# Performance work log

Measured on AMD Instinct MI355X. Metric: run time of the kernel, lower is better.

Reference implementation:

```python
import jax, jax.numpy as jnp
import numpy as np

N = 100000
E = 3200000
IN_C, HID_C, OUT_C = 128, 128, 64


def setup_inputs() -> dict:
    key = jax.random.key(0)
    k_x, k_e, k_w1, k_w2 = jax.random.split(key, 4)
    x = jax.random.normal(k_x, (N, IN_C), dtype=jnp.float32)
    edge_index = jax.random.randint(k_e, (2, E), 0, N, dtype=jnp.int64)
    # GCNConv uses Glorot-init weight [in, out] and zero bias
    W1 = jax.random.normal(k_w1, (IN_C, HID_C), dtype=jnp.float32) * (1.0 / np.sqrt(IN_C))
    b1 = jnp.zeros((HID_C,), dtype=jnp.float32)
    W2 = jax.random.normal(k_w2, (HID_C, OUT_C), dtype=jnp.float32) * (1.0 / np.sqrt(HID_C))
    b2 = jnp.zeros((OUT_C,), dtype=jnp.float32)
    return {"x": x, "edge_index": edge_index, "W1": W1, "b1": b1, "W2": W2, "b2": b2}


def _gcn_norm(edge_index, n_nodes):
    """Add self-loops and compute symmetric normalization coefficients."""
    loop = jnp.arange(n_nodes, dtype=edge_index.dtype)
    src = jnp.concatenate([edge_index[0], loop])  # [E+N]
    dst = jnp.concatenate([edge_index[1], loop])  # [E+N]
    ones = jnp.ones(src.shape[0], dtype=jnp.float32)
    deg = jax.ops.segment_sum(ones, dst, num_segments=n_nodes)  # in-degree w/ self loops
    dinv = jnp.where(deg > 0, jax.lax.rsqrt(deg), 0.0)
    norm = dinv[src] * dinv[dst]  # [E+N]
    return src, dst, norm


def _gcn_conv(x, W, b, src, dst, norm, n_nodes):
    h = x @ W                                   # [N, out] dense transform first (PyG order)
    msg = norm[:, None] * h[src]                # gather + scale  [E+N, out]
    out = jax.ops.segment_sum(msg, dst, num_segments=n_nodes)  # scatter-add
    return out + b


def reference(x, edge_index, W1, b1, W2, b2):
    src, dst, norm = _gcn_norm(edge_index, N)
    h = _gcn_conv(x, W1, b1, src, dst, norm, N)
    h = jax.nn.relu(h)
    out = _gcn_conv(h, W2, b2, src, dst, norm, N)
    return out
```

## Files before the change

### kernel.cpp

```cpp
#include <hip/hip_runtime.h>

typedef unsigned int u32;
typedef unsigned short u16;
typedef unsigned long long u64;
typedef __bf16 bf16x8 __attribute__((ext_vector_type(8)));
typedef float floatx4 __attribute__((ext_vector_type(4)));
typedef u32 u32x2 __attribute__((ext_vector_type(2)));
typedef u32 u32x4 __attribute__((ext_vector_type(4)));
typedef float floatx2 __attribute__((ext_vector_type(2)));

__device__ __forceinline__ u16 f2bf(float f) {
  u32 u = __float_as_uint(f);
  u += 0x7fffu + ((u >> 16) & 1u);
  return (u16)(u >> 16);
}
__device__ __forceinline__ float bflo(u32 v) { return __uint_as_float(v << 16); }
__device__ __forceinline__ float bfhi(u32 v) { return __uint_as_float(v & 0xffff0000u); }

#define SLICE_SH 10
#define SL (1 << SLICE_SH)
#define MAXNS 128
#define NBBIN 1280

__global__ void probe_dtypes(const u16* __restrict__ xs, const u32* __restrict__ eis,
                             int* __restrict__ flags, int* __restrict__ scur) {
  int lane = threadIdx.x;
  if (lane < MAXNS) scur[lane] = 0;
  if (lane >= 64) return;
  int big = 0;
  for (int i = lane; i < 4096; i += 64) {
    u32 e = (xs[i] >> 7) & 0xffu;
    big += (e >= 0xC0u) ? 1 : 0;
  }
  int odd = 0;
  for (int i = lane; i < 256; i += 64)
    odd += (eis[2 * i + 1] != 0u) ? 1 : 0;
#pragma unroll
  for (int off = 32; off; off >>= 1) {
    big += __shfl_down(big, off);
    odd += __shfl_down(odd, off);
  }
  if (lane == 0 && blockIdx.x == 0) {
    flags[0] = (big > 16) ? 1 : 0;
    flags[1] = (odd == 0) ? 1 : 0;
  }
}


template <int OUT, bool XPROBED>
__device__ __forceinline__ void gemm_body(const void* __restrict__ Xv,
                                          const void* __restrict__ Wv,
                                          const int* __restrict__ flags,
                                          u16* __restrict__ Y, int nrows,
                                          int bid, u16* Wt) {
  constexpr int K = 128;
  constexpr int NT = OUT / 16;
  constexpr int LDW = K + 8;
  const int wf32 = flags[0];
  const int xf32 = XPROBED ? wf32 : 0;
  int tid = threadIdx.x;
  if (wf32) {
    const float* Wf = (const float*)Wv;
    for (int idx = tid; idx < K * OUT; idx += 256) {
      int k = idx / OUT, n = idx % OUT;
      Wt[n * LDW + k] = f2bf(Wf[idx]);
    }
  } else {
    const u16* Wu = (const u16*)Wv;
    for (int idx = tid; idx < K * OUT; idx += 256) {
      int k = idx / OUT, n = idx % OUT;
      Wt[n * LDW + k] = Wu[idx];
    }
  }
  __syncthreads();
  int lane = tid & 63, wave = tid >> 6;
  int quad = lane >> 4, low = lane & 15;
  int mBase = bid * 64 + wave * 16;
  int m = mBase + low;
  int ml = (m < nrows) ? m : (nrows - 1);
  floatx4 acc[NT];
#pragma unroll
  for (int i = 0; i < NT; i++) acc[i] = (floatx4)0.0f;
#pragma unroll
  for (int kb = 0; kb < 4; kb++) {
    int k0 = kb * 32 + quad * 8;
    bf16x8 a;
    if (xf32) {
      const float* Xf = (const float*)Xv;
      floatx4 p0 = *(const floatx4*)(Xf + (size_t)ml * K + k0);
      floatx4 p1 = *(const floatx4*)(Xf + (size_t)ml * K + k0 + 4);
      union { bf16x8 v; u16 s[8]; } au;
#pragma unroll
      for (int j = 0; j < 4; j++) { au.s[j] = f2bf(p0[j]); au.s[4 + j] = f2bf(p1[j]); }
      a = au.v;
    } else {
      a = *(const bf16x8*)((const u16*)Xv + (size_t)ml * K + k0);
    }
#pragma unroll
    for (int nt = 0; nt < NT; nt++) {
      bf16x8 b = *(const bf16x8*)(&Wt[(nt * 16 + low) * LDW + k0]);
      acc[nt] = __builtin_amdgcn_mfma_f32_16x16x32_bf16(a, b, acc[nt], 0, 0, 0);
    }
  }
#pragma unroll
  for (int nt = 0; nt < NT; nt++) {
    int col = nt * 16 + low;
#pragma unroll
    for (int r = 0; r < 4; r++) {
      int row = mBase + quad * 4 + r;
      if (row < nrows) Y[(size_t)row * OUT + col] = f2bf(acc[nt][r]);
    }
  }
}

__device__ __forceinline__ void bin_body(const int* __restrict__ ei,
                                         const int* __restrict__ flags,
                                         int* __restrict__ scur,
                                         u64* __restrict__ stA, u64* __restrict__ stB,
                                         int splitS, int cap, int e, int ns,
                                         int bid, int* hist, int* curs) {
  int per = (e + NBBIN - 1) / NBBIN;
  int e0 = bid * per;
  int e1 = e0 + per; if (e1 > e) e1 = e;
  const int i64f = flags[1];
  for (int t = threadIdx.x; t < ns; t += 256) hist[t] = 0;
  __syncthreads();
  for (int i = e0 + threadIdx.x; i < e1; i += 256) {
    int d = i64f ? ei[2 * (e + i)] : ei[e + i];
    atomicAdd(&hist[d >> SLICE_SH], 1);
  }
  __syncthreads();
  for (int t = threadIdx.x; t < ns; t += 256)
    curs[t] = atomicAdd(&scur[t], hist[t]);
  __syncthreads();
  int i = e0 + threadIdx.x;
  for (; i + 768 < e1; i += 1024) {
    int d[4], s[4], pos[4];
#pragma unroll
    for (int p = 0; p < 4; p++) {
      int ii = i + 256 * p;
      if (i64f) { s[p] = ei[2 * ii]; d[p] = ei[2 * (e + ii)]; }
      else      { s[p] = ei[ii];     d[p] = ei[e + ii]; }
    }
#pragma unroll
    for (int p = 0; p < 4; p++) pos[p] = atomicAdd(&curs[d[p] >> SLICE_SH], 1);
#pragma unroll
    for (int p = 0; p < 4; p++) {
      int sl = d[p] >> SLICE_SH;
      u64* st = (sl < splitS) ? stA + (size_t)sl * cap : stB + (size_t)(sl - splitS) * cap;
      st[pos[p]] = ((u64)(u32)d[p] << 32) | (u32)s[p];
    }
  }
  for (; i < e1; i += 256) {
    int s, d;
    if (i64f) { s = ei[2 * i]; d = ei[2 * (e + i)]; }
    else      { s = ei[i];     d = ei[e + i]; }
    int sl = d >> SLICE_SH;
    u64* st = (sl < splitS) ? stA + (size_t)sl * cap : stB + (size_t)(sl - splitS) * cap;
    st[atomicAdd(&curs[sl], 1)] = ((u64)(u32)d << 32) | (u32)s;
  }
}

__global__ __launch_bounds__(256) void gemm1_bin(const void* __restrict__ Xv,
                                                 const void* __restrict__ Wv,
                                                 const int* __restrict__ flags,
                                                 u16* __restrict__ Y, int nrows, int nbGemm,
                                                 const int* __restrict__ ei,
                                                 int* __restrict__ scur,
                                                 u64* __restrict__ stA, u64* __restrict__ stB,
                                                 int splitS, int cap, int e, int ns) {
  __shared__ __attribute__((aligned(16))) char smbuf[128 * 136 * 2];
  int id = blockIdx.x;
  int small = (NBBIN < nbGemm) ? NBBIN : nbGemm;
  int isBin, bid;
  if (id < 2 * small) { isBin = !(id & 1); bid = id >> 1; }
  else { bid = small + (id - 2 * small); isBin = (NBBIN > nbGemm); }
  if (isBin) {
    int* hist = (int*)smbuf;
    int* curs = hist + MAXNS;
    bin_body(ei, flags, scur, stA, stB, splitS, cap, e, ns, bid, hist, curs);
  } else {
    gemm_body<128, true>(Xv, Wv, flags, Y, nrows, bid, (u16*)smbuf);
  }
}

__global__ __launch_bounds__(256) void gemm2_k(const void* __restrict__ Xv,
                                               const void* __restrict__ Wv,
                                               const int* __restrict__ flags,
                                               u16* __restrict__ Y, int nrows) {
  __shared__ u16 Wt[64 * 136];
  gemm_body<64, false>(Xv, Wv, flags, Y, nrows, blockIdx.x, Wt);
}

__global__ __launch_bounds__(1024) void fill_slice3(const u64* __restrict__ stA,
                                                    const u64* __restrict__ stB,
                                                    const int* __restrict__ scur,
                                                    int* __restrict__ rp,
                                                    float* __restrict__ dinv,
                                                    int* __restrict__ csr,
                                                    int splitS, int cap, int n, int ns) {
  __shared__ int cnt[SL];
  __shared__ int part[SL];
  __shared__ int sb[MAXNS];
  const int s = blockIdx.x;
  const int base = s << SLICE_SH;
  const int tid = threadIdx.x;
  cnt[tid] = 0;
  if (tid < MAXNS) sb[tid] = (tid < ns) ? scur[tid] : 0;
  __syncthreads();
  for (int off = 1; off < MAXNS; off <<= 1) {
    int v = 0;
    if (tid < MAXNS && tid >= off) v = sb[tid - off];
    __syncthreads();
    if (tid < MAXNS) sb[tid] += v;
    __syncthreads();
  }
  const int csrLo = s ? sb[s - 1] : 0;
  const int m = sb[s] - csrLo;
  if (s == ns - 1 && tid == 0) rp[n] = sb[ns - 1];
  const u64* st = (s < splitS) ? stA + (size_t)s * cap : stB + (size_t)(s - splitS) * cap;
  {
    int i = tid;
    for (; i + 7168 < m; i += 8192) {
      int b[8];
#pragma unroll
      for (int p = 0; p < 8; p++) b[p] = (int)(st[i + 1024 * p] >> 32) & (SL - 1);
#pragma unroll
      for (int p = 0; p < 8; p++) atomicAdd(&cnt[b[p]], 1);
    }
    for (; i < m; i += 1024)
      atomicAdd(&cnt[(int)(st[i] >> 32) & (SL - 1)], 1);
  }
  __syncthreads();
  int c0 = cnt[tid];
  part[tid] = c0;
  __syncthreads();
  for (int off = 1; off < SL; off <<= 1) {
    int t = (tid >= off) ? part[tid - off] : 0;
    __syncthreads();
    part[tid] += t;
    __syncthreads();
  }
  int p0 = csrLo + (tid ? part[tid - 1] : 0);
  __syncthreads();
  cnt[tid] = p0;
  int d0 = base + tid;
  if (d0 < n) { rp[d0] = p0; dinv[d0] = rsqrtf((float)(c0 + 1)); }
  __syncthreads();
  {
    int i = tid;
    for (; i + 7168 < m; i += 8192) {
      u64 pr[8]; int pos[8];
#pragma unroll
      for (int p = 0; p < 8; p++) pr[p] = st[i + 1024 * p];
#pragma unroll
      for (int p = 0; p < 8; p++)
        pos[p] = atomicAdd(&cnt[(int)(pr[p] >> 32) & (SL - 1)], 1);
#pragma unroll
      for (int p = 0; p < 8; p++) csr[pos[p]] = (int)(pr[p] & 0xffffffffu);
    }
    for (; i < m; i += 1024) {
      u64 pr = st[i];
      int pos = atomicAdd(&cnt[(int)(pr >> 32) & (SL - 1)], 1);
      csr[pos] = (int)(pr & 0xffffffffu);
    }
  }
}


__global__ __launch_bounds__(256) void agg_128(const u32* __restrict__ H,
                                               const int* __restrict__ rp,
                                               const int* __restrict__ cs,
                                               const float* __restrict__ dinv,
                                               const void* __restrict__ biasv,
                                               const int* __restrict__ flags,
                                               u32* __restrict__ out, int n) {
  int node = blockIdx.x * 4 + (threadIdx.x >> 6);
  if (node >= n) return;
  int lane = threadIdx.x & 63;
  int e4 = lane >> 4, c = lane & 15;
  int s0 = rp[node], s1 = rp[node + 1];
  float a[8] = {0.f, 0.f, 0.f, 0.f, 0.f, 0.f, 0.f, 0.f};
  for (int base = s0; base < s1; base += 64) {
    int nb = s1 - base; if (nb > 64) nb = 64;
    int src = 0; float dv = 0.f;
    if (lane < nb) { src = cs[base + lane]; dv = dinv[src]; }
    for (int j = 0; j < nb; j += 16) {
      u32x4 v[4]; float w[4];
#pragma unroll
      for (int p = 0; p < 4; p++) {
        int idx = j + 4 * p + e4;
        int sj = __shfl(src, idx);
        w[p] = __shfl(dv, idx);
        v[p] = *(const u32x4*)(H + (size_t)sj * 64 + 4 * c);
      }
#pragma unroll
      for (int p = 0; p < 4; p++) {
#pragma unroll
        for (int k = 0; k < 4; k++) {
          a[2 * k]     += w[p] * bflo(v[p][k]);
          a[2 * k + 1] += w[p] * bfhi(v[p][k]);
        }
      }
    }
  }
#pragma unroll
  for (int k = 0; k < 8; k++) {
    a[k] += __shfl_xor(a[k], 16);
    a[k] += __shfl_xor(a[k], 32);
  }
  float ds = dinv[node];
  u32x4 vs = *(const u32x4*)(H + (size_t)node * 64 + 4 * c);
  float r[8];
#pragma unroll
  for (int k = 0; k < 4; k++) {
    r[2 * k]     = ds * (a[2 * k]     + ds * bflo(vs[k]));
    r[2 * k + 1] = ds * (a[2 * k + 1] + ds * bfhi(vs[k]));
  }
  if (flags[0]) {
    floatx4 b0 = *(const floatx4*)((const float*)biasv + 8 * c);
    floatx4 b1 = *(const floatx4*)((const float*)biasv + 8 * c + 4);
#pragma unroll
    for (int k = 0; k < 4; k++) { r[k] += b0[k]; r[4 + k] += b1[k]; }
  } else {
    u32x4 bb = *(const u32x4*)((const u32*)biasv + 4 * c);
#pragma unroll
    for (int k = 0; k < 4; k++) { r[2 * k] += bflo(bb[k]); r[2 * k + 1] += bfhi(bb[k]); }
  }
#pragma unroll
  for (int k = 0; k < 8; k++) r[k] = fmaxf(r[k], 0.f);
  if (e4 == 0) {
    u32x4 o;
#pragma unroll
    for (int k = 0; k < 4; k++)
      o[k] = (u32)f2bf(r[2 * k]) | ((u32)f2bf(r[2 * k + 1]) << 16);
    *(u32x4*)(out + (size_t)node * 64 + 4 * c) = o;
  }
}

__global__ __launch_bounds__(256) void agg_64(const u16* __restrict__ Hu,
                                              const int* __restrict__ rp,
                                              const int* __restrict__ cs,
                                              const float* __restrict__ dinv,
                                              const void* __restrict__ biasv,
                                              const int* __restrict__ flags,
                                              void* __restrict__ outv, int n) {
  const u32* H = (const u32*)Hu;
  int node = blockIdx.x * 4 + (threadIdx.x >> 6);
  if (node >= n) return;
  int lane = threadIdx.x & 63;
  int e4 = lane >> 4, c = lane & 15;
  int s0 = rp[node], s1 = rp[node + 1];
  float a[4] = {0.f, 0.f, 0.f, 0.f};
  for (int base = s0; base < s1; base += 64) {
    int nb = s1 - base; if (nb > 64) nb = 64;
    int src = 0; float dv = 0.f;
    if (lane < nb) { src = cs[base + lane]; dv = dinv[src]; }
    for (int j = 0; j < nb; j += 16) {
      u32x2 v[4]; float w[4];
#pragma unroll
      for (int p = 0; p < 4; p++) {
        int idx = j + 4 * p + e4;
        int sj = __shfl(src, idx);
        w[p] = __shfl(dv, idx);
        v[p] = *(const u32x2*)(H + (size_t)sj * 32 + 2 * c);
      }
#pragma unroll
      for (int p = 0; p < 4; p++) {
        a[0] += w[p] * bflo(v[p].x); a[1] += w[p] * bfhi(v[p].x);
        a[2] += w[p] * bflo(v[p].y); a[3] += w[p] * bfhi(v[p].y);
      }
    }
  }
#pragma unroll
  for (int k = 0; k < 4; k++) {
    a[k] += __shfl_xor(a[k], 16);
    a[k] += __shfl_xor(a[k], 32);
  }
  float ds = dinv[node];
  u32x2 vs = *(const u32x2*)(H + (size_t)node * 32 + 2 * c);
  float r0 = ds * (a[0] + ds * bflo(vs.x));
  float r1 = ds * (a[1] + ds * bfhi(vs.x));
  float r2 = ds * (a[2] + ds * bflo(vs.y));
  float r3 = ds * (a[3] + ds * bfhi(vs.y));
  if (flags[0]) {
    floatx4 bf = *(const floatx4*)((const float*)biasv + 4 * c);
    r0 += bf[0]; r1 += bf[1]; r2 += bf[2]; r3 += bf[3];
    if (e4 == 0) {
      floatx4 o; o[0] = r0; o[1] = r1; o[2] = r2; o[3] = r3;
      *(floatx4*)((float*)outv + (size_t)node * 64 + 4 * c) = o;
    }
  } else {
    u32x2 bb = *(const u32x2*)((const u32*)biasv + 2 * c);
    r0 += bflo(bb.x); r1 += bfhi(bb.x); r2 += bflo(bb.y); r3 += bfhi(bb.y);
    if (e4 == 0) {
      u32x2 o;
      o.x = (u32)f2bf(r0) | ((u32)f2bf(r1) << 16);
      o.y = (u32)f2bf(r2) | ((u32)f2bf(r3) << 16);
      *(u32x2*)((u32*)outv + (size_t)node * 32 + 2 * c) = o;
    }
  }
}


extern "C" void kernel_launch(void* const* d_in, const int* in_sizes, int n_in,
                              void* d_out, int out_size, void* d_ws, size_t ws_size,
                              hipStream_t stream) {
  const void* x  = d_in[0];
  const int*  ei = (const int*)d_in[1];
  const void* W1 = d_in[2];
  const void* b1 = d_in[3];
  const void* W2 = d_in[4];
  const void* b2 = d_in[5];
  const int N = in_sizes[0] / 128;
  const int E = in_sizes[1] / 2;
  const int NS = (N + SL - 1) >> SLICE_SH;

  int CAP = (E + NS - 1) / NS;
  CAP += CAP / 8;
  size_t doutSlots = ((size_t)out_size * 2) / 8;
  int SPLIT = (int)(doutSlots / (size_t)CAP);
  if (SPLIT > NS) SPLIT = NS;

  auto al = [](size_t v) { return (v + 255) & ~(size_t)255; };
  char* ws = (char*)d_ws;
  size_t o = 0;
  int*   flags = (int*)(ws + o);  o += 256;
  int*   scur  = (int*)(ws + o);  o += 512;
  int*   rp    = (int*)(ws + o);  o += al((size_t)(N + 1) * 4);
  float* dinv  = (float*)(ws + o); o += al((size_t)N * 4);
  int*   csr   = (int*)(ws + o);  o += al((size_t)E * 4);
  u16*   h     = (u16*)(ws + o);  o += al((size_t)N * 128 * 2);
  u16*   h1    = (u16*)(ws + o);  o += al((size_t)N * 128 * 2);
  u16*   h2    = h;
  u64* stA = (u64*)d_out;
  u64* stB = (u64*)h1;

  const int nbGemm = (N + 63) / 64;

  probe_dtypes<<<1, 128, 0, stream>>>((const u16*)x, (const u32*)ei, flags, scur);
  gemm1_bin<<<NBBIN + nbGemm, 256, 0, stream>>>(x, W1, flags, h, N, nbGemm,
                                                ei, scur, stA, stB, SPLIT, CAP, E, NS);
  fill_slice3<<<NS, 1024, 0, stream>>>(stA, stB, scur, rp, dinv, csr, SPLIT, CAP, N, NS);
  agg_128<<<(N + 3) / 4, 256, 0, stream>>>((const u32*)h, rp, csr, dinv, b1, flags, (u32*)h1, N);
  gemm2_k<<<nbGemm, 256, 0, stream>>>(h1, W2, flags, h2, N);
  agg_64<<<(N + 3) / 4, 256, 0, stream>>>(h2, rp, csr, dinv, b2, flags, d_out, N);
}
```

Before: 384.2 us.

## Fuse second GEMM into layer-1 aggregation and drop runtime dtype probing

The layer-1 aggregation kernel now applies bias and ReLU, packs the 4 per-block node rows into LDS, and multiplies them by W2 with MFMA directly. This removes the separate gemm2 kernel and the h1 round trip through global memory. The dtype-probe kernel and its flag branches are removed: inputs are assumed to be fp32, edges int32, and the output fp32, and a memset replaces the counter reset. In exchange, every 4-node block reloads and converts all of W2 into LDS. The 16-row MFMA tile also carries only 4 valid rows, which adds substantial redundant work per block.

```diff
diff --git a/kernel.cpp b/kernel.cpp
--- a/kernel.cpp
+++ b/kernel.cpp
@@ -7,7 +7,7 @@
 typedef float floatx4 __attribute__((ext_vector_type(4)));
 typedef u32 u32x2 __attribute__((ext_vector_type(2)));
 typedef u32 u32x4 __attribute__((ext_vector_type(4)));
-typedef float floatx2 __attribute__((ext_vector_type(2)));
+
 
 __device__ __forceinline__ u16 f2bf(float f) {
   u32 u = __float_as_uint(f);
@@ -22,55 +22,15 @@
 #define MAXNS 128
 #define NBBIN 1280
 
-__global__ void probe_dtypes(const u16* __restrict__ xs, const u32* __restrict__ eis,
-                             int* __restrict__ flags, int* __restrict__ scur) {
-  int lane = threadIdx.x;
-  if (lane < MAXNS) scur[lane] = 0;
-  if (lane >= 64) return;
-  int big = 0;
-  for (int i = lane; i < 4096; i += 64) {
-    u32 e = (xs[i] >> 7) & 0xffu;
-    big += (e >= 0xC0u) ? 1 : 0;
-  }
-  int odd = 0;
-  for (int i = lane; i < 256; i += 64)
-    odd += (eis[2 * i + 1] != 0u) ? 1 : 0;
-#pragma unroll
-  for (int off = 32; off; off >>= 1) {
-    big += __shfl_down(big, off);
-    odd += __shfl_down(odd, off);
-  }
-  if (lane == 0 && blockIdx.x == 0) {
-    flags[0] = (big > 16) ? 1 : 0;
-    flags[1] = (odd == 0) ? 1 : 0;
-  }
-}
-
-
-template <int OUT, bool XPROBED>
-__device__ __forceinline__ void gemm_body(const void* __restrict__ Xv,
-                                          const void* __restrict__ Wv,
-                                          const int* __restrict__ flags,
-                                          u16* __restrict__ Y, int nrows,
-                                          int bid, u16* Wt) {
-  constexpr int K = 128;
-  constexpr int NT = OUT / 16;
-  constexpr int LDW = K + 8;
-  const int wf32 = flags[0];
-  const int xf32 = XPROBED ? wf32 : 0;
+__device__ __forceinline__ void gemm1_body(const float* __restrict__ X,
+                                           const float* __restrict__ W,
+                                           u16* __restrict__ Y, int nrows,
+                                           int bid, u16* Wt) {
+  constexpr int K = 128, OUT = 128, NT = 8, LDW = 136;
   int tid = threadIdx.x;
-  if (wf32) {
-    const float* Wf = (const float*)Wv;
-    for (int idx = tid; idx < K * OUT; idx += 256) {
-      int k = idx / OUT, n = idx % OUT;
-      Wt[n * LDW + k] = f2bf(Wf[idx]);
-    }
-  } else {
-    const u16* Wu = (const u16*)Wv;
-    for (int idx = tid; idx < K * OUT; idx += 256) {
-      int k = idx / OUT, n = idx % OUT;
-      Wt[n * LDW + k] = Wu[idx];
-    }
+  for (int idx = tid; idx < K * OUT; idx += 256) {
+    int k = idx >> 7, n = idx & 127;
+    Wt[n * LDW + k] = f2bf(W[idx]);
   }
   __syncthreads();
   int lane = tid & 63, wave = tid >> 6;
@@ -84,22 +44,15 @@
 #pragma unroll
   for (int kb = 0; kb < 4; kb++) {
     int k0 = kb * 32 + quad * 8;
-    bf16x8 a;
-    if (xf32) {
-      const float* Xf = (const float*)Xv;
-      floatx4 p0 = *(const floatx4*)(Xf + (size_t)ml * K + k0);
-      floatx4 p1 = *(const floatx4*)(Xf + (size_t)ml * K + k0 + 4);
-      union { bf16x8 v; u16 s[8]; } au;
-#pragma unroll
-      for (int j = 0; j < 4; j++) { au.s[j] = f2bf(p0[j]); au.s[4 + j] = f2bf(p1[j]); }
-      a = au.v;
-    } else {
-      a = *(const bf16x8*)((const u16*)Xv + (size_t)ml * K + k0);
-    }
+    floatx4 p0 = *(const floatx4*)(X + (size_t)ml * K + k0);
+    floatx4 p1 = *(const floatx4*)(X + (size_t)ml * K + k0 + 4);
+    union { bf16x8 v; u16 s[8]; } au;
+#pragma unroll
+    for (int j = 0; j < 4; j++) { au.s[j] = f2bf(p0[j]); au.s[4 + j] = f2bf(p1[j]); }
 #pragma unroll
     for (int nt = 0; nt < NT; nt++) {
       bf16x8 b = *(const bf16x8*)(&Wt[(nt * 16 + low) * LDW + k0]);
-      acc[nt] = __builtin_amdgcn_mfma_f32_16x16x32_bf16(a, b, acc[nt], 0, 0, 0);
+      acc[nt] = __builtin_amdgcn_mfma_f32_16x16x32_bf16(au.v, b, acc[nt], 0, 0, 0);
     }
   }
 #pragma unroll
@@ -114,7 +67,6 @@
 }
 
 __device__ __forceinline__ void bin_body(const int* __restrict__ ei,
-                                         const int* __restrict__ flags,
                                          int* __restrict__ scur,
                                          u64* __restrict__ stA, u64* __restrict__ stB,
                                          int splitS, int cap, int e, int ns,
@@ -122,11 +74,10 @@
   int per = (e + NBBIN - 1) / NBBIN;
   int e0 = bid * per;
   int e1 = e0 + per; if (e1 > e) e1 = e;
-  const int i64f = flags[1];
   for (int t = threadIdx.x; t < ns; t += 256) hist[t] = 0;
   __syncthreads();
   for (int i = e0 + threadIdx.x; i < e1; i += 256) {
-    int d = i64f ? ei[2 * (e + i)] : ei[e + i];
+    int d = ei[e + i];
     atomicAdd(&hist[d >> SLICE_SH], 1);
   }
   __syncthreads();
@@ -139,8 +90,7 @@
 #pragma unroll
     for (int p = 0; p < 4; p++) {
       int ii = i + 256 * p;
-      if (i64f) { s[p] = ei[2 * ii]; d[p] = ei[2 * (e + ii)]; }
-      else      { s[p] = ei[ii];     d[p] = ei[e + ii]; }
+      s[p] = ei[ii]; d[p] = ei[e + ii];
     }
 #pragma unroll
     for (int p = 0; p < 4; p++) pos[p] = atomicAdd(&curs[d[p] >> SLICE_SH], 1);
@@ -152,18 +102,15 @@
     }
   }
   for (; i < e1; i += 256) {
-    int s, d;
-    if (i64f) { s = ei[2 * i]; d = ei[2 * (e + i)]; }
-    else      { s = ei[i];     d = ei[e + i]; }
+    int s = ei[i], d = ei[e + i];
     int sl = d >> SLICE_SH;
     u64* st = (sl < splitS) ? stA + (size_t)sl * cap : stB + (size_t)(sl - splitS) * cap;
     st[atomicAdd(&curs[sl], 1)] = ((u64)(u32)d << 32) | (u32)s;
   }
 }
 
-__global__ __launch_bounds__(256) void gemm1_bin(const void* __restrict__ Xv,
-                                                 const void* __restrict__ Wv,
-                                                 const int* __restrict__ flags,
+__global__ __launch_bounds__(256) void gemm1_bin(const float* __restrict__ X,
+                                                 const float* __restrict__ W1,
                                                  u16* __restrict__ Y, int nrows, int nbGemm,
                                                  const int* __restrict__ ei,
                                                  int* __restrict__ scur,
@@ -178,18 +125,10 @@
   if (isBin) {
     int* hist = (int*)smbuf;
     int* curs = hist + MAXNS;
-    bin_body(ei, flags, scur, stA, stB, splitS, cap, e, ns, bid, hist, curs);
+    bin_body(ei, scur, stA, stB, splitS, cap, e, ns, bid, hist, curs);
   } else {
-    gemm_body<128, true>(Xv, Wv, flags, Y, nrows, bid, (u16*)smbuf);
-  }
-}
-
-__global__ __launch_bounds__(256) void gemm2_k(const void* __restrict__ Xv,
-                                               const void* __restrict__ Wv,
-                                               const int* __restrict__ flags,
-                                               u16* __restrict__ Y, int nrows) {
-  __shared__ u16 Wt[64 * 136];
-  gemm_body<64, false>(Xv, Wv, flags, Y, nrows, blockIdx.x, Wt);
+    gemm1_body(X, W1, Y, nrows, bid, (u16*)smbuf);
+  }
 }
 
 __global__ __launch_bounds__(1024) void fill_slice3(const u64* __restrict__ stA,
@@ -267,19 +206,26 @@
   }
 }
 
-
-__global__ __launch_bounds__(256) void agg_128(const u32* __restrict__ H,
-                                               const int* __restrict__ rp,
-                                               const int* __restrict__ cs,
-                                               const float* __restrict__ dinv,
-                                               const void* __restrict__ biasv,
-                                               const int* __restrict__ flags,
-                                               u32* __restrict__ out, int n) {
-  int node = blockIdx.x * 4 + (threadIdx.x >> 6);
-  if (node >= n) return;
-  int lane = threadIdx.x & 63;
+__global__ __launch_bounds__(256) void agg128_g2(const u32* __restrict__ H,
+                                                 const int* __restrict__ rp,
+                                                 const int* __restrict__ cs,
+                                                 const float* __restrict__ dinv,
+                                                 const float* __restrict__ b1,
+                                                 const float* __restrict__ W2,
+                                                 u16* __restrict__ h2, int n) {
+  __shared__ u16 Wt[64 * 136];
+  __shared__ u16 Arow[16 * 136];
+  const int tid = threadIdx.x;
+  for (int idx = tid; idx < 128 * 64; idx += 256) {
+    int k = idx >> 6, nn = idx & 63;
+    Wt[nn * 136 + k] = f2bf(W2[idx]);
+  }
+  const int nodeBase = blockIdx.x * 4;
+  const int wave = tid >> 6, lane = tid & 63;
+  int node = nodeBase + wave;
+  int nodeC = (node < n) ? node : (n - 1);
   int e4 = lane >> 4, c = lane & 15;
-  int s0 = rp[node], s1 = rp[node + 1];
+  int s0 = rp[nodeC], s1 = rp[nodeC + 1];
   float a[8] = {0.f, 0.f, 0.f, 0.f, 0.f, 0.f, 0.f, 0.f};
   for (int base = s0; base < s1; base += 64) {
     int nb = s1 - base; if (nb > 64) nb = 64;
@@ -309,32 +255,42 @@
     a[k] += __shfl_xor(a[k], 16);
     a[k] += __shfl_xor(a[k], 32);
   }
-  float ds = dinv[node];
-  u32x4 vs = *(const u32x4*)(H + (size_t)node * 64 + 4 * c);
+  float ds = dinv[nodeC];
+  u32x4 vs = *(const u32x4*)(H + (size_t)nodeC * 64 + 4 * c);
+  floatx4 bb0 = *(const floatx4*)(b1 + 8 * c);
+  floatx4 bb1 = *(const floatx4*)(b1 + 8 * c + 4);
   float r[8];
 #pragma unroll
   for (int k = 0; k < 4; k++) {
     r[2 * k]     = ds * (a[2 * k]     + ds * bflo(vs[k]));
     r[2 * k + 1] = ds * (a[2 * k + 1] + ds * bfhi(vs[k]));
   }
-  if (flags[0]) {
-    floatx4 b0 = *(const floatx4*)((const float*)biasv + 8 * c);
-    floatx4 b1 = *(const floatx4*)((const float*)biasv + 8 * c + 4);
-#pragma unroll
-    for (int k = 0; k < 4; k++) { r[k] += b0[k]; r[4 + k] += b1[k]; }
-  } else {
-    u32x4 bb = *(const u32x4*)((const u32*)biasv + 4 * c);
-#pragma unroll
-    for (int k = 0; k < 4; k++) { r[2 * k] += bflo(bb[k]); r[2 * k + 1] += bfhi(bb[k]); }
-  }
+#pragma unroll
+  for (int k = 0; k < 4; k++) { r[k] += bb0[k]; r[4 + k] += bb1[k]; }
 #pragma unroll
   for (int k = 0; k < 8; k++) r[k] = fmaxf(r[k], 0.f);
   if (e4 == 0) {
-    u32x4 o;
-#pragma unroll
-    for (int k = 0; k < 4; k++)
-      o[k] = (u32)f2bf(r[2 * k]) | ((u32)f2bf(r[2 * k + 1]) << 16);
-    *(u32x4*)(out + (size_t)node * 64 + 4 * c) = o;
+    union { u16 s[8]; u32x4 v; } pk;
+#pragma unroll
+    for (int k = 0; k < 8; k++) pk.s[k] = f2bf(r[k]);
+    *(u32x4*)&Arow[wave * 136 + 8 * c] = pk.v;
+  }
+  __syncthreads();
+  const int quad = e4, low = c;
+  floatx4 acc = (floatx4)0.0f;
+#pragma unroll
+  for (int kb = 0; kb < 4; kb++) {
+    int k0 = kb * 32 + quad * 8;
+    bf16x8 af = *(const bf16x8*)&Arow[low * 136 + k0];
+    bf16x8 bf = *(const bf16x8*)&Wt[(wave * 16 + low) * 136 + k0];
+    acc = __builtin_amdgcn_mfma_f32_16x16x32_bf16(af, bf, acc, 0, 0, 0);
+  }
+  if (quad == 0) {
+#pragma unroll
+    for (int rI = 0; rI < 4; rI++) {
+      int row = nodeBase + rI;
+      if (row < n) h2[(size_t)row * 64 + wave * 16 + low] = f2bf(acc[rI]);
+    }
   }
 }
 
@@ -342,9 +298,8 @@
                                               const int* __restrict__ rp,
                                               const int* __restrict__ cs,
                                               const float* __restrict__ dinv,
-                                              const void* __restrict__ biasv,
-                                              const int* __restrict__ flags,
-                                              void* __restrict__ outv, int n) {
+                                              const float* __restrict__ b2,
+                                              float* __restrict__ out, int n) {
   const u32* H = (const u32*)Hu;
   int node = blockIdx.x * 4 + (threadIdx.x >> 6);
   if (node >= n) return;
@@ -379,26 +334,14 @@
   }
   float ds = dinv[node];
   u32x2 vs = *(const u32x2*)(H + (size_t)node * 32 + 2 * c);
-  float r0 = ds * (a[0] + ds * bflo(vs.x));
-  float r1 = ds * (a[1] + ds * bfhi(vs.x));
-  float r2 = ds * (a[2] + ds * bflo(vs.y));
-  float r3 = ds * (a[3] + ds * bfhi(vs.y));
-  if (flags[0]) {
-    floatx4 bf = *(const floatx4*)((const float*)biasv + 4 * c);
-    r0 += bf[0]; r1 += bf[1]; r2 += bf[2]; r3 += bf[3];
-    if (e4 == 0) {
-      floatx4 o; o[0] = r0; o[1] = r1; o[2] = r2; o[3] = r3;
-      *(floatx4*)((float*)outv + (size_t)node * 64 + 4 * c) = o;
-    }
-  } else {
-    u32x2 bb = *(const u32x2*)((const u32*)biasv + 2 * c);
-    r0 += bflo(bb.x); r1 += bfhi(bb.x); r2 += bflo(bb.y); r3 += bfhi(bb.y);
-    if (e4 == 0) {
-      u32x2 o;
-      o.x = (u32)f2bf(r0) | ((u32)f2bf(r1) << 16);
-      o.y = (u32)f2bf(r2) | ((u32)f2bf(r3) << 16);
-      *(u32x2*)((u32*)outv + (size_t)node * 32 + 2 * c) = o;
-    }
+  floatx4 bf = *(const floatx4*)(b2 + 4 * c);
+  if (e4 == 0) {
+    floatx4 o;
+    o[0] = ds * (a[0] + ds * bflo(vs.x)) + bf[0];
+    o[1] = ds * (a[1] + ds * bfhi(vs.x)) + bf[1];
+    o[2] = ds * (a[2] + ds * bflo(vs.y)) + bf[2];
+    o[3] = ds * (a[3] + ds * bfhi(vs.y)) + bf[3];
+    *(floatx4*)(out + (size_t)node * 64 + 4 * c) = o;
   }
 }
 
@@ -406,43 +349,40 @@
 extern "C" void kernel_launch(void* const* d_in, const int* in_sizes, int n_in,
                               void* d_out, int out_size, void* d_ws, size_t ws_size,
                               hipStream_t stream) {
-  const void* x  = d_in[0];
-  const int*  ei = (const int*)d_in[1];
-  const void* W1 = d_in[2];
-  const void* b1 = d_in[3];
-  const void* W2 = d_in[4];
-  const void* b2 = d_in[5];
+  const float* x  = (const float*)d_in[0];
+  const int*   ei = (const int*)d_in[1];
+  const float* W1 = (const float*)d_in[2];
+  const float* b1 = (const float*)d_in[3];
+  const float* W2 = (const float*)d_in[4];
+  const float* b2 = (const float*)d_in[5];
   const int N = in_sizes[0] / 128;
   const int E = in_sizes[1] / 2;
   const int NS = (N + SL - 1) >> SLICE_SH;
 
   int CAP = (E + NS - 1) / NS;
   CAP += CAP / 8;
-  size_t doutSlots = ((size_t)out_size * 2) / 8;
+  size_t doutSlots = ((size_t)out_size * 4) / 8;
   int SPLIT = (int)(doutSlots / (size_t)CAP);
   if (SPLIT > NS) SPLIT = NS;
 
   auto al = [](size_t v) { return (v + 255) & ~(size_t)255; };
   char* ws = (char*)d_ws;
   size_t o = 0;
-  int*   flags = (int*)(ws + o);  o += 256;
   int*   scur  = (int*)(ws + o);  o += 512;
   int*   rp    = (int*)(ws + o);  o += al((size_t)(N + 1) * 4);
   float* dinv  = (float*)(ws + o); o += al((size_t)N * 4);
   int*   csr   = (int*)(ws + o);  o += al((size_t)E * 4);
   u16*   h     = (u16*)(ws + o);  o += al((size_t)N * 128 * 2);
-  u16*   h1    = (u16*)(ws + o);  o += al((size_t)N * 128 * 2);
-  u16*   h2    = h;
+  u16*   h2    = (u16*)(ws + o);  o += al((size_t)N * 128 * 2);
   u64* stA = (u64*)d_out;
-  u64* stB = (u64*)h1;
+  u64* stB = (u64*)h2;
 
   const int nbGemm = (N + 63) / 64;
 
-  probe_dtypes<<<1, 128, 0, stream>>>((const u16*)x, (const u32*)ei, flags, scur);
-  gemm1_bin<<<NBBIN + nbGemm, 256, 0, stream>>>(x, W1, flags, h, N, nbGemm,
+  hipMemsetAsync(scur, 0, 512, stream);
+  gemm1_bin<<<NBBIN + nbGemm, 256, 0, stream>>>(x, W1, h, N, nbGemm,
                                                 ei, scur, stA, stB, SPLIT, CAP, E, NS);
   fill_slice3<<<NS, 1024, 0, stream>>>(stA, stB, scur, rp, dinv, csr, SPLIT, CAP, N, NS);
-  agg_128<<<(N + 3) / 4, 256, 0, stream>>>((const u32*)h, rp, csr, dinv, b1, flags, (u32*)h1, N);
-  gemm2_k<<<nbGemm, 256, 0, stream>>>(h1, W2, flags, h2, N);
-  agg_64<<<(N + 3) / 4, 256, 0, stream>>>(h2, rp, csr, dinv, b2, flags, d_out, N);
-}
+  agg128_g2<<<(N + 3) / 4, 256, 0, stream>>>((const u32*)h, rp, csr, dinv, b1, W2, h2, N);
+  agg_64<<<(N + 3) / 4, 256, 0, stream>>>(h2, rp, csr, dinv, b2, (float*)d_out, N);
+}
```

New measurement: 381.6 us. No clear change (-0.7%).
